# Optimization experiments

Measured on AMD Instinct MI355X. Metric: run time of the kernel, lower is better.

The kernel has to match this reference:

```python
import jax, jax.numpy as jnp
import numpy as np

LOG2 = float(np.log(2.0))

def ssp(x):
    # shifted softplus: log(0.5*exp(x) + 0.5)
    return jax.nn.softplus(x) - LOG2


def setup_inputs() -> dict:
    B, A, N = 8, 512, 64
    n_atom, n_spatial, n_filters = 256, 128, 256
    n_ang_feat = 2 * 2 * 2 * 8 * 2  # 2*n_zetas*2*n_angular*n_zetas = 128
    key = jax.random.key(0)
    ks = jax.random.split(key, 16)
    f32 = jnp.float32
    inp = {
        'x': jax.random.normal(ks[0], (B, A, n_atom), f32),
        'r_ij': jax.random.uniform(ks[1], (B, A, N), f32) * 6.0,  # some beyond cutoff=5
        'f_ij': jax.random.normal(ks[2], (B, A, N, n_spatial), f32),
        'G_i': jax.random.normal(ks[3], (B, A, n_ang_feat), f32),
        'neighbor_mask': jnp.ones((B, A, N), f32),
        'neighbors': jax.random.randint(ks[4], (B, A, N), 0, A),
        # CFConv params: in2f (no bias), filter MLP, f2out
        'W_in2f': jax.random.normal(ks[5], (n_atom, n_filters), f32) * (n_atom ** -0.5),
        'W1': jax.random.normal(ks[6], (n_spatial, n_filters), f32) * (n_spatial ** -0.5),
        'b1': jnp.zeros((n_filters,), f32),
        'W2': jax.random.normal(ks[7], (n_filters, n_filters), f32) * (n_filters ** -0.5),
        'b2': jnp.zeros((n_filters,), f32),
        'W_f2out': jax.random.normal(ks[8], (n_filters, n_atom), f32) * (n_filters ** -0.5),
        'b_f2out': jnp.zeros((n_atom,), f32),
        # post-cfconv dense and angular dense (no bias)
        'W_dense': jax.random.normal(ks[9], (n_atom, n_atom), f32) * (n_atom ** -0.5),
        'b_dense': jnp.zeros((n_atom,), f32),
        'W_ang': jax.random.normal(ks[10], (n_ang_feat, n_atom), f32) * (n_ang_feat ** -0.5),
    }
    return inp


def reference(x, r_ij, f_ij, G_i, neighbor_mask, neighbors,
              W_in2f, W1, b1, W2, b2, W_f2out, b_f2out,
              W_dense, b_dense, W_ang):
    cutoff = 5.0
    # filter-generating MLP on distance expansion: [B,A,N,n_filters]
    W = ssp(jnp.einsum('bans,sf->banf', f_ij, W1) + b1)
    W = jnp.einsum('banf,fg->bang', W, W2) + b2
    # hard cutoff mask on distances
    C = (r_ij <= cutoff).astype(W.dtype)
    W = W * C[..., None]
    # in2f projection then neighbor gather
    xf = jnp.einsum('bad,df->baf', x, W_in2f)  # [B,A,F]
    B, A, F = xf.shape
    N = neighbors.shape[-1]
    y = jnp.take_along_axis(xf, neighbors.reshape(B, A * N, 1), axis=1)
    y = y.reshape(B, A, N, F)
    # elementwise filter, mask padded neighbors, sum-aggregate over neighbors
    y = (y * W * neighbor_mask[..., None]).sum(axis=2)  # [B,A,F]
    v_rad = jnp.einsum('baf,fd->bad', y, W_f2out) + b_f2out
    v_rad = jnp.einsum('bad,de->bae', v_rad, W_dense) + b_dense
    v_ang = jnp.einsum('bag,gd->bad', G_i, W_ang)
    return ssp(v_rad + v_ang)
```

## Files before the change

### kernel.cpp

```cpp
#include <hip/hip_runtime.h>


typedef __bf16 bf16x8 __attribute__((ext_vector_type(8)));
typedef float f32x4 __attribute__((ext_vector_type(4)));
typedef unsigned short u16;
typedef unsigned int u32;

#define LDA 136
#define LDH 264

static __device__ __forceinline__ float b2f(u16 u) {
  union { float f; u32 i; } v; v.i = ((u32)u) << 16; return v.f;
}
static __device__ __forceinline__ u32 rndb(float f) {
  u32 u = __builtin_bit_cast(u32, f);
  return u + 0x7fffu + ((u >> 16) & 1u);
}
static __device__ __forceinline__ u16 f2b(float f) { return (u16)(rndb(f) >> 16); }
static __device__ __forceinline__ u32 pk2(float lo, float hi) {
  return __builtin_amdgcn_perm(rndb(hi), rndb(lo), 0x07060302);
}
static __device__ __forceinline__ float sspf(float x) {
  float t = __expf(-fabsf(x));
  return fmaxf(x, 0.0f) + __logf(1.0f + t) - 0.6931471805599453f;
}
static __device__ __forceinline__ bf16x8 ldfrag(const u16* p) {
  return __builtin_bit_cast(bf16x8, *(const uint4*)p);
}
static __device__ __forceinline__ float ldsc(const u16* p, bool fm, size_t i) {
  return fm ? ((const float*)p)[i] : b2f(p[i]);
}

static __device__ __forceinline__ void pack_strip(
    const u16* __restrict__ W, bool fm, int q, int KC, u16* __restrict__ dst, u16* T) {
  int tid = threadIdx.x;
  if (fm) {
    const float* src = (const float*)W + (size_t)q * 32 * 256;
#pragma unroll
    for (int i = 0; i < 8; i++) {
      int c = tid + 256 * i;
      int row = c >> 6, col4 = (c & 63) * 4;
      float4 v = *(const float4*)(src + (size_t)row * 256 + col4);
      uint2 o; o.x = pk2(v.x, v.y); o.y = pk2(v.z, v.w);
      *(uint2*)(T + row * LDH + col4) = o;
    }
  } else {
    const u16* src = W + (size_t)q * 32 * 256;
#pragma unroll
    for (int i = 0; i < 8; i++) {
      int c = tid + 256 * i;
      int row = c >> 6, col4 = (c & 63) * 4;
      *(uint2*)(T + row * LDH + col4) = *(const uint2*)(src + (size_t)row * 256 + col4);
    }
  }
  __syncthreads();
#pragma unroll
  for (int i = 0; i < 4; i++) {
    int idx = tid + 256 * i;
    int flane = idx & 63, c = idx >> 6;
    int col = c * 16 + (flane & 15);
    int r0 = (flane >> 4) * 8;
    u32 t0 = (u32)T[(r0 + 0) * LDH + col] | ((u32)T[(r0 + 1) * LDH + col] << 16);
    u32 t1 = (u32)T[(r0 + 2) * LDH + col] | ((u32)T[(r0 + 3) * LDH + col] << 16);
    u32 t2 = (u32)T[(r0 + 4) * LDH + col] | ((u32)T[(r0 + 5) * LDH + col] << 16);
    u32 t3 = (u32)T[(r0 + 6) * LDH + col] | ((u32)T[(r0 + 7) * LDH + col] << 16);
    uint4 o; o.x = t0; o.y = t1; o.z = t2; o.w = t3;
    *(uint4*)(dst + ((size_t)(c * KC + q) * 64 + flane) * 8) = o;
  }
}

__global__ __launch_bounds__(256) void pack_win(
    const u16* __restrict__ Win, const u16* __restrict__ nm, u16* __restrict__ outb) {
  __shared__ __align__(16) u16 T[32 * LDH];
  pack_strip(Win, nm[0] == 0, blockIdx.x, 8, outb + 1048576, T);
}

__global__ __launch_bounds__(256) void pack5(
    const u16* __restrict__ W1, const u16* __restrict__ W2, const u16* __restrict__ Wf,
    const u16* __restrict__ Wd, const u16* __restrict__ Wa,
    const u16* __restrict__ nm, u16* __restrict__ dst) {
  __shared__ __align__(16) u16 T[32 * LDH];
  bool fm = (nm[0] == 0);
  int b = blockIdx.x;
  if (b < 4)       pack_strip(W1, fm, b,      4, dst,          T);
  else if (b < 12) pack_strip(W2, fm, b - 4,  8, dst + 32768,  T);
  else if (b < 20) pack_strip(Wf, fm, b - 12, 8, dst + 98304,  T);
  else if (b < 28) pack_strip(Wd, fm, b - 20, 8, dst + 163840, T);
  else             pack_strip(Wa, fm, b - 28, 4, dst + 229376, T);
}

__global__ __launch_bounds__(256) void k1_xf(
    const u16* __restrict__ x, const u16* __restrict__ nm, u16* __restrict__ outb) {
  __shared__ __align__(16) u16 sX[16 * LDH];
  bool fm = (nm[0] == 0);
  int bid = blockIdx.x, tid = threadIdx.x;
  int w = tid >> 6, lane = tid & 63, quad = lane >> 4, l16 = lane & 15;
  if (fm) {
    const float* src = (const float*)x + (size_t)bid * 4096;
#pragma unroll
    for (int i = 0; i < 2; i++) {
      int c = tid + 256 * i;
      float4 a = *(const float4*)(src + c * 8), b = *(const float4*)(src + c * 8 + 4);
      uint4 o; o.x = pk2(a.x, a.y); o.y = pk2(a.z, a.w);
      o.z = pk2(b.x, b.y); o.w = pk2(b.z, b.w);
      *(uint4*)(sX + (c >> 5) * LDH + (c & 31) * 8) = o;
    }
  } else {
    const u16* src = x + (size_t)bid * 4096;
#pragma unroll
    for (int i = 0; i < 2; i++) {
      int c = tid + 256 * i;
      *(uint4*)(sX + (c >> 5) * LDH + (c & 31) * 8) = *(const uint4*)(src + c * 8);
    }
  }
  __syncthreads();
  const u16* winp = outb + 1048576;
  f32x4 acc[4];
#pragma unroll
  for (int ct = 0; ct < 4; ct++) acc[ct] = (f32x4){0.f, 0.f, 0.f, 0.f};
#pragma unroll
  for (int q = 0; q < 8; q++) {
    bf16x8 af = ldfrag(sX + l16 * LDH + q * 32 + quad * 8);
    bf16x8 bfr[4];
#pragma unroll
    for (int ct = 0; ct < 4; ct++)
      bfr[ct] = ldfrag(winp + ((size_t)((w * 4 + ct) * 8 + q) * 64 + lane) * 8);
#pragma unroll
    for (int ct = 0; ct < 4; ct++)
      acc[ct] = __builtin_amdgcn_mfma_f32_16x16x32_bf16(af, bfr[ct], acc[ct], 0, 0, 0);
  }
#pragma unroll
  for (int ct = 0; ct < 4; ct++) {
    int f = w * 64 + ct * 16 + l16;
#pragma unroll
    for (int r = 0; r < 4; r++)
      outb[(size_t)(bid * 16 + quad * 4 + r) * 256 + f] = f2b(acc[ct][r]);
  }
}

__global__ __launch_bounds__(256, 3) void k2_main(
    u16* __restrict__ fij, const u16* __restrict__ rij, const u16* __restrict__ nm,
    const int* __restrict__ nbr, const u16* __restrict__ b1, const u16* __restrict__ b2,
    const u16* __restrict__ packed, const u16* __restrict__ xf) {
  __shared__ __align__(16) u16 sF[64 * LDA];
  __shared__ __align__(16) u16 sH[64 * LDH];
  __shared__ float cm[64];
  __shared__ int nb[64];
  bool fm = (nm[0] == 0);
  const u16* w1p = packed;
  const u16* w2p = packed + 32768;
  int bid = blockIdx.x, tid = threadIdx.x;
  int w = tid >> 6, lane = tid & 63, quad = lane >> 4, l16 = lane & 15;

  if (fm) {
    const float* fsrc = (const float*)fij + (size_t)bid * 8192;
#pragma unroll
    for (int i = 0; i < 4; i++) {
      int c = tid + 256 * i;
      const float* p = fsrc + c * 8;
      float4 a = *(const float4*)p, b = *(const float4*)(p + 4);
      uint4 o; o.x = pk2(a.x, a.y); o.y = pk2(a.z, a.w);
      o.z = pk2(b.x, b.y); o.w = pk2(b.z, b.w);
      *(uint4*)(sF + (c >> 4) * LDA + (c & 15) * 8) = o;
    }
  } else {
    const u16* fsrc = fij + (size_t)bid * 8192;
#pragma unroll
    for (int i = 0; i < 4; i++) {
      int c = tid + 256 * i;
      *(uint4*)(sF + (c >> 4) * LDA + (c & 15) * 8) = *(const uint4*)(fsrc + c * 8);
    }
  }
  if (tid < 64) {
    float r = ldsc(rij, fm, (size_t)bid * 64 + tid);
    float m = ldsc(nm, fm, (size_t)bid * 64 + tid);
    cm[tid] = (r <= 5.0f) ? m : 0.0f;
    nb[tid] = nbr[bid * 64 + tid];
  }
  __syncthreads();

  f32x4 zero = {0.f, 0.f, 0.f, 0.f};
  f32x4 acc[4][4];
#pragma unroll
  for (int mt = 0; mt < 4; mt++)
#pragma unroll
    for (int ct = 0; ct < 4; ct++) acc[mt][ct] = zero;
#pragma unroll
  for (int q = 0; q < 4; q++) {
    bf16x8 af[4], bfr[4];
#pragma unroll
    for (int mt = 0; mt < 4; mt++)
      af[mt] = ldfrag(sF + (mt * 16 + l16) * LDA + q * 32 + quad * 8);
#pragma unroll
    for (int ct = 0; ct < 4; ct++)
      bfr[ct] = ldfrag(w1p + ((size_t)((w * 4 + ct) * 4 + q) * 64 + lane) * 8);
#pragma unroll
    for (int mt = 0; mt < 4; mt++)
#pragma unroll
      for (int ct = 0; ct < 4; ct++)
        acc[mt][ct] = __builtin_amdgcn_mfma_f32_16x16x32_bf16(af[mt], bfr[ct], acc[mt][ct], 0, 0, 0);
  }
  float bb1[4];
#pragma unroll
  for (int ct = 0; ct < 4; ct++) bb1[ct] = ldsc(b1, fm, w * 64 + ct * 16 + l16);
#pragma unroll
  for (int ct = 0; ct < 4; ct++) {
    int f = w * 64 + ct * 16 + l16;
#pragma unroll
    for (int mt = 0; mt < 4; mt++)
#pragma unroll
      for (int r = 0; r < 4; r++)
        sH[(mt * 16 + quad * 4 + r) * LDH + f] = f2b(sspf(acc[mt][ct][r] + bb1[ct]));
  }
  __syncthreads();

  f32x4 acc2[4][4];
#pragma unroll
  for (int mt = 0; mt < 4; mt++)
#pragma unroll
    for (int ct = 0; ct < 4; ct++) acc2[mt][ct] = zero;
#pragma unroll 2
  for (int q = 0; q < 8; q++) {
    bf16x8 af[4], bfr[4];
#pragma unroll
    for (int mt = 0; mt < 4; mt++)
      af[mt] = ldfrag(sH + (mt * 16 + l16) * LDH + q * 32 + quad * 8);
#pragma unroll
    for (int ct = 0; ct < 4; ct++)
      bfr[ct] = ldfrag(w2p + ((size_t)((w * 4 + ct) * 8 + q) * 64 + lane) * 8);
#pragma unroll
    for (int mt = 0; mt < 4; mt++)
#pragma unroll
      for (int ct = 0; ct < 4; ct++)
        acc2[mt][ct] = __builtin_amdgcn_mfma_f32_16x16x32_bf16(af[mt], bfr[ct], acc2[mt][ct], 0, 0, 0);
  }
  __syncthreads();

  float bb2[4];
#pragma unroll
  for (int ct = 0; ct < 4; ct++) bb2[ct] = ldsc(b2, fm, w * 64 + ct * 16 + l16);
#pragma unroll
  for (int ct = 0; ct < 4; ct++) {
    int f = w * 64 + ct * 16 + l16;
#pragma unroll
    for (int mt = 0; mt < 4; mt++)
#pragma unroll
      for (int r = 0; r < 4; r++) {
        int m = mt * 16 + quad * 4 + r;
        sH[m * LDH + f] = f2b((acc2[mt][ct][r] + bb2[ct]) * cm[m]);
      }
  }
  __syncthreads();

  {
    int f = tid;
    int b_of = (bid >> 9) * 512;
    const u16* xb = xf + f;
    float s = 0.0f;
#pragma unroll 8
    for (int m = 0; m < 64; m++) {
      float wv = b2f(sH[m * LDH + f]);
      float xv = b2f(xb[(size_t)(b_of + nb[m]) * 256]);
      s += wv * xv;
    }
    size_t yoff = (size_t)bid * (fm ? 16384 : 8192);
    fij[yoff + f] = f2b(s);
  }
}

__global__ __launch_bounds__(256, 3) void k3_out(
    const u16* __restrict__ fij, const u16* __restrict__ G, const u16* __restrict__ bf2,
    const u16* __restrict__ bd, const u16* __restrict__ nm,
    const u16* __restrict__ packed, u16* __restrict__ outb) {
  __shared__ __align__(16) u16 sY[32 * LDH];
  __shared__ __align__(16) u16 sH2[32 * LDH];
  __shared__ __align__(16) u16 sG[32 * LDA];
  bool fm = (nm[0] == 0);
  const u16* wfp = packed + 98304;
  const u16* wdp = packed + 163840;
  const u16* wap = packed + 229376;
  int bid = blockIdx.x, tid = threadIdx.x;
  int w = tid >> 6, lane = tid & 63, quad = lane >> 4, l16 = lane & 15;
  size_t ystr = fm ? 16384 : 8192;
#pragma unroll
  for (int i = 0; i < 4; i++) {
    int c = tid + 256 * i;
    int row = c >> 5;
    const u16* src = fij + (size_t)(bid * 32 + row) * ystr + (c & 31) * 8;
    *(uint4*)(sY + row * LDH + (c & 31) * 8) = *(const uint4*)src;
  }
  if (fm) {
    const float* g32 = (const float*)G;
#pragma unroll
    for (int i = 0; i < 2; i++) {
      int c = tid + 256 * i;
      int row = c >> 4;
      const float* p = g32 + (size_t)(bid * 32 + row) * 128 + (c & 15) * 8;
      float4 a = *(const float4*)p, b = *(const float4*)(p + 4);
      uint4 o; o.x = pk2(a.x, a.y); o.y = pk2(a.z, a.w);
      o.z = pk2(b.x, b.y); o.w = pk2(b.z, b.w);
      *(uint4*)(sG + row * LDA + (c & 15) * 8) = o;
    }
  } else {
#pragma unroll
    for (int i = 0; i < 2; i++) {
      int c = tid + 256 * i;
      int row = c >> 4;
      *(uint4*)(sG + row * LDA + (c & 15) * 8) =
          *(const uint4*)(G + (size_t)(bid * 32 + row) * 128 + (c & 15) * 8);
    }
  }
  __syncthreads();
  f32x4 zero = {0.f, 0.f, 0.f, 0.f};
  f32x4 acc[2][4];
#pragma unroll
  for (int mt = 0; mt < 2; mt++)
#pragma unroll
    for (int ct = 0; ct < 4; ct++) acc[mt][ct] = zero;
#pragma unroll
  for (int q = 0; q < 8; q++) {
    bf16x8 af[2], bfr[4];
#pragma unroll
    for (int mt = 0; mt < 2; mt++)
      af[mt] = ldfrag(sY + (mt * 16 + l16) * LDH + q * 32 + quad * 8);
#pragma unroll
    for (int ct = 0; ct < 4; ct++)
      bfr[ct] = ldfrag(wfp + ((size_t)((w * 4 + ct) * 8 + q) * 64 + lane) * 8);
#pragma unroll
    for (int mt = 0; mt < 2; mt++)
#pragma unroll
      for (int ct = 0; ct < 4; ct++)
        acc[mt][ct] = __builtin_amdgcn_mfma_f32_16x16x32_bf16(af[mt], bfr[ct], acc[mt][ct], 0, 0, 0);
  }
#pragma unroll
  for (int ct = 0; ct < 4; ct++) {
    int f = w * 64 + ct * 16 + l16;
    float bb = ldsc(bf2, fm, f);
#pragma unroll
    for (int mt = 0; mt < 2; mt++)
#pragma unroll
      for (int r = 0; r < 4; r++)
        sH2[(mt * 16 + quad * 4 + r) * LDH + f] = f2b(acc[mt][ct][r] + bb);
  }
  __syncthreads();
#pragma unroll
  for (int mt = 0; mt < 2; mt++)
#pragma unroll
    for (int ct = 0; ct < 4; ct++) acc[mt][ct] = zero;
#pragma unroll
  for (int q = 0; q < 8; q++) {
    bf16x8 af[2], bfr[4];
#pragma unroll
    for (int mt = 0; mt < 2; mt++)
      af[mt] = ldfrag(sH2 + (mt * 16 + l16) * LDH + q * 32 + quad * 8);
#pragma unroll
    for (int ct = 0; ct < 4; ct++)
      bfr[ct] = ldfrag(wdp + ((size_t)((w * 4 + ct) * 8 + q) * 64 + lane) * 8);
#pragma unroll
    for (int mt = 0; mt < 2; mt++)
#pragma unroll
      for (int ct = 0; ct < 4; ct++)
        acc[mt][ct] = __builtin_amdgcn_mfma_f32_16x16x32_bf16(af[mt], bfr[ct], acc[mt][ct], 0, 0, 0);
  }
#pragma unroll
  for (int q = 0; q < 4; q++) {
    bf16x8 af[2], bfr[4];
#pragma unroll
    for (int mt = 0; mt < 2; mt++)
      af[mt] = ldfrag(sG + (mt * 16 + l16) * LDA + q * 32 + quad * 8);
#pragma unroll
    for (int ct = 0; ct < 4; ct++)
      bfr[ct] = ldfrag(wap + ((size_t)((w * 4 + ct) * 4 + q) * 64 + lane) * 8);
#pragma unroll
    for (int mt = 0; mt < 2; mt++)
#pragma unroll
      for (int ct = 0; ct < 4; ct++)
        acc[mt][ct] = __builtin_amdgcn_mfma_f32_16x16x32_bf16(af[mt], bfr[ct], acc[mt][ct], 0, 0, 0);
  }
  float* out32 = (float*)outb;
#pragma unroll
  for (int ct = 0; ct < 4; ct++) {
    int f = w * 64 + ct * 16 + l16;
    float bb = ldsc(bd, fm, f);
#pragma unroll
    for (int mt = 0; mt < 2; mt++)
#pragma unroll
      for (int r = 0; r < 4; r++) {
        int m = mt * 16 + quad * 4 + r;
        float v = sspf(acc[mt][ct][r] + bb);
        size_t idx = ((size_t)bid * 32 + m) * 256 + f;
        if (fm) out32[idx] = v; else outb[idx] = f2b(v);
      }
  }
}

extern "C" void kernel_launch(void* const* d_in, const int* in_sizes, int n_in,
                              void* d_out, int out_size, void* d_ws, size_t ws_size,
                              hipStream_t stream) {
  u16*       x    = (u16*)d_in[0];
  const u16* rij  = (const u16*)d_in[1];
  u16*       fij  = (u16*)d_in[2];
  const u16* Gi   = (const u16*)d_in[3];
  const u16* nmsk = (const u16*)d_in[4];
  const int* nbr  = (const int*)d_in[5];
  const u16* Win  = (const u16*)d_in[6];
  const u16* W1   = (const u16*)d_in[7];
  const u16* b1   = (const u16*)d_in[8];
  const u16* W2   = (const u16*)d_in[9];
  const u16* b2   = (const u16*)d_in[10];
  const u16* Wf   = (const u16*)d_in[11];
  const u16* bf2  = (const u16*)d_in[12];
  const u16* Wd   = (const u16*)d_in[13];
  const u16* bd   = (const u16*)d_in[14];
  const u16* Wa   = (const u16*)d_in[15];
  u16* out = (u16*)d_out;

  pack_win<<<8, 256, 0, stream>>>(Win, nmsk, out);
  k1_xf<<<256, 256, 0, stream>>>(x, nmsk, out);
  pack5<<<32, 256, 0, stream>>>(W1, W2, Wf, Wd, Wa, nmsk, x);
  k2_main<<<4096, 256, 0, stream>>>(fij, rij, nmsk, nbr, b1, b2, x, out);
  k3_out<<<128, 256, 0, stream>>>(fij, Gi, bf2, bd, nmsk, x, out);
}
```

Measured before the change: 311.2 us.

## Fuse filter epilogue with neighbor aggregation in registers and regroup weight packing

```diff
diff --git a/kernel.cpp b/kernel.cpp
--- a/kernel.cpp
+++ b/kernel.cpp
@@ -2,7 +2,9 @@
 
 
 typedef __bf16 bf16x8 __attribute__((ext_vector_type(8)));
+typedef __bf16 bf16x2 __attribute__((ext_vector_type(2)));
 typedef float f32x4 __attribute__((ext_vector_type(4)));
+typedef int i32x4 __attribute__((ext_vector_type(4)));
 typedef unsigned short u16;
 typedef unsigned int u32;
 
@@ -12,17 +14,16 @@
 static __device__ __forceinline__ float b2f(u16 u) {
   union { float f; u32 i; } v; v.i = ((u32)u) << 16; return v.f;
 }
-static __device__ __forceinline__ u32 rndb(float f) {
-  u32 u = __builtin_bit_cast(u32, f);
-  return u + 0x7fffu + ((u >> 16) & 1u);
-}
-static __device__ __forceinline__ u16 f2b(float f) { return (u16)(rndb(f) >> 16); }
+static __device__ __forceinline__ u16 f2b(float f) {
+  return __builtin_bit_cast(u16, (__bf16)f);
+}
 static __device__ __forceinline__ u32 pk2(float lo, float hi) {
-  return __builtin_amdgcn_perm(rndb(hi), rndb(lo), 0x07060302);
+  bf16x2 v; v[0] = (__bf16)lo; v[1] = (__bf16)hi;
+  return __builtin_bit_cast(u32, v);
 }
 static __device__ __forceinline__ float sspf(float x) {
-  float t = __expf(-fabsf(x));
-  return fmaxf(x, 0.0f) + __logf(1.0f + t) - 0.6931471805599453f;
+  float t = __expf(fminf(x, 60.0f));
+  return __logf(fmaf(t, 0.5f, 0.5f));
 }
 static __device__ __forceinline__ bf16x8 ldfrag(const u16* p) {
   return __builtin_bit_cast(bf16x8, *(const uint4*)p);
@@ -69,24 +70,26 @@
   }
 }
 
-__global__ __launch_bounds__(256) void pack_win(
-    const u16* __restrict__ Win, const u16* __restrict__ nm, u16* __restrict__ outb) {
+__global__ __launch_bounds__(256) void pack_a(
+    const u16* __restrict__ Win, const u16* __restrict__ W1, const u16* __restrict__ W2,
+    const u16* __restrict__ nm, u16* __restrict__ outb) {
   __shared__ __align__(16) u16 T[32 * LDH];
-  pack_strip(Win, nm[0] == 0, blockIdx.x, 8, outb + 1048576, T);
-}
-
-__global__ __launch_bounds__(256) void pack5(
-    const u16* __restrict__ W1, const u16* __restrict__ W2, const u16* __restrict__ Wf,
-    const u16* __restrict__ Wd, const u16* __restrict__ Wa,
+  bool fm = (nm[0] == 0);
+  int b = blockIdx.x;
+  if (b < 8)       pack_strip(Win, fm, b,      8, outb + 1048576, T);
+  else if (b < 12) pack_strip(W1,  fm, b - 8,  4, outb + 1114112, T);
+  else             pack_strip(W2,  fm, b - 12, 8, outb + 1146880, T);
+}
+
+__global__ __launch_bounds__(256) void pack_b(
+    const u16* __restrict__ Wf, const u16* __restrict__ Wd, const u16* __restrict__ Wa,
     const u16* __restrict__ nm, u16* __restrict__ dst) {
   __shared__ __align__(16) u16 T[32 * LDH];
   bool fm = (nm[0] == 0);
   int b = blockIdx.x;
-  if (b < 4)       pack_strip(W1, fm, b,      4, dst,          T);
-  else if (b < 12) pack_strip(W2, fm, b - 4,  8, dst + 32768,  T);
-  else if (b < 20) pack_strip(Wf, fm, b - 12, 8, dst + 98304,  T);
-  else if (b < 28) pack_strip(Wd, fm, b - 20, 8, dst + 163840, T);
-  else             pack_strip(Wa, fm, b - 28, 4, dst + 229376, T);
+  if (b < 8)       pack_strip(Wf, fm, b,      8, dst + 98304,  T);
+  else if (b < 16) pack_strip(Wd, fm, b - 8,  8, dst + 163840, T);
+  else             pack_strip(Wa, fm, b - 16, 4, dst + 229376, T);
 }
 
 __global__ __launch_bounds__(256) void k1_xf(
@@ -141,14 +144,14 @@
 __global__ __launch_bounds__(256, 3) void k2_main(
     u16* __restrict__ fij, const u16* __restrict__ rij, const u16* __restrict__ nm,
     const int* __restrict__ nbr, const u16* __restrict__ b1, const u16* __restrict__ b2,
-    const u16* __restrict__ packed, const u16* __restrict__ xf) {
+    const u16* __restrict__ xf) {
   __shared__ __align__(16) u16 sF[64 * LDA];
   __shared__ __align__(16) u16 sH[64 * LDH];
-  __shared__ float cm[64];
-  __shared__ int nb[64];
+  __shared__ __align__(16) float cm[64];
+  __shared__ __align__(16) int nb[64];
   bool fm = (nm[0] == 0);
-  const u16* w1p = packed;
-  const u16* w2p = packed + 32768;
+  const u16* w1p = xf + 1114112;
+  const u16* w2p = xf + 1146880;
   int bid = blockIdx.x, tid = threadIdx.x;
   int w = tid >> 6, lane = tid & 63, quad = lane >> 4, l16 = lane & 15;
 
@@ -234,37 +237,35 @@
       for (int ct = 0; ct < 4; ct++)
         acc2[mt][ct] = __builtin_amdgcn_mfma_f32_16x16x32_bf16(af[mt], bfr[ct], acc2[mt][ct], 0, 0, 0);
   }
-  __syncthreads();
 
   float bb2[4];
 #pragma unroll
   for (int ct = 0; ct < 4; ct++) bb2[ct] = ldsc(b2, fm, w * 64 + ct * 16 + l16);
+  int b_of = (bid >> 9) * 512;
+  float s[4] = {0.f, 0.f, 0.f, 0.f};
+#pragma unroll
+  for (int mt = 0; mt < 4; mt++) {
+    f32x4 cmv = *(const f32x4*)(cm + mt * 16 + quad * 4);
+    i32x4 nbv = *(const i32x4*)(nb + mt * 16 + quad * 4);
+#pragma unroll
+    for (int r = 0; r < 4; r++) {
+      const u16* xrow = xf + (size_t)(b_of + nbv[r]) * 256 + w * 64 + l16;
+      float c = cmv[r];
+#pragma unroll
+      for (int ct = 0; ct < 4; ct++)
+        s[ct] = fmaf((acc2[mt][ct][r] + bb2[ct]) * c, b2f(xrow[ct * 16]), s[ct]);
+    }
+  }
 #pragma unroll
   for (int ct = 0; ct < 4; ct++) {
-    int f = w * 64 + ct * 16 + l16;
-#pragma unroll
-    for (int mt = 0; mt < 4; mt++)
-#pragma unroll
-      for (int r = 0; r < 4; r++) {
-        int m = mt * 16 + quad * 4 + r;
-        sH[m * LDH + f] = f2b((acc2[mt][ct][r] + bb2[ct]) * cm[m]);
-      }
-  }
-  __syncthreads();
-
-  {
-    int f = tid;
-    int b_of = (bid >> 9) * 512;
-    const u16* xb = xf + f;
-    float s = 0.0f;
-#pragma unroll 8
-    for (int m = 0; m < 64; m++) {
-      float wv = b2f(sH[m * LDH + f]);
-      float xv = b2f(xb[(size_t)(b_of + nb[m]) * 256]);
-      s += wv * xv;
-    }
+    s[ct] += __shfl_xor(s[ct], 16);
+    s[ct] += __shfl_xor(s[ct], 32);
+  }
+  if (quad == 0) {
     size_t yoff = (size_t)bid * (fm ? 16384 : 8192);
-    fij[yoff + f] = f2b(s);
+#pragma unroll
+    for (int ct = 0; ct < 4; ct++)
+      fij[yoff + w * 64 + ct * 16 + l16] = f2b(s[ct]);
   }
 }
 
@@ -415,9 +416,9 @@
   const u16* Wa   = (const u16*)d_in[15];
   u16* out = (u16*)d_out;
 
-  pack_win<<<8, 256, 0, stream>>>(Win, nmsk, out);
+  pack_a<<<20, 256, 0, stream>>>(Win, W1, W2, nmsk, out);
   k1_xf<<<256, 256, 0, stream>>>(x, nmsk, out);
-  pack5<<<32, 256, 0, stream>>>(W1, W2, Wf, Wd, Wa, nmsk, x);
-  k2_main<<<4096, 256, 0, stream>>>(fij, rij, nmsk, nbr, b1, b2, x, out);
+  pack_b<<<20, 256, 0, stream>>>(Wf, Wd, Wa, nmsk, x);
+  k2_main<<<4096, 256, 0, stream>>>(fij, rij, nmsk, nbr, b1, b2, out);
   k3_out<<<128, 256, 0, stream>>>(fij, Gi, bf2, bd, nmsk, x, out);
 }
```

New measurement: 293.6 us. -5.7%, faster.
